# Kernel optimization log

Measured on AMD Instinct MI355X. Metric: run time of the kernel, lower is better.

The kernel has to match this reference:

```python
import jax, jax.numpy as jnp
import numpy as np

D_MODEL = 512
DK = 4
DV = 8
HIDD = 10
HEAD = D_MODEL // DV  # 64
LN_EPS = 1e-5


def setup_inputs() -> dict:
    key = jax.random.key(0)
    ks = jax.random.split(key, 10)
    B, S, Se = 8, 512, 512
    u = jax.random.uniform  # torch.rand initializer for attention weights
    n = jax.random.normal
    return {
        "x": n(ks[0], (B, S, D_MODEL), jnp.float32),
        "x_enc": n(ks[1], (B, Se, D_MODEL), jnp.float32),
        "WqM": u(ks[2], (D_MODEL, HEAD * DK), jnp.float32),
        "WkM": u(ks[3], (D_MODEL, HEAD * DK), jnp.float32),
        "WvM": u(ks[4], (D_MODEL, HEAD * DV), jnp.float32),
        "ln_g": jnp.ones((D_MODEL,), jnp.float32),
        "ln_b": jnp.zeros((D_MODEL,), jnp.float32),
        "fc1_w": n(ks[5], (HIDD, D_MODEL), jnp.float32) * (1.0 / np.sqrt(D_MODEL)),
        "fc1_b": jnp.zeros((HIDD,), jnp.float32),
        "fc2_w": n(ks[6], (D_MODEL, HIDD), jnp.float32) * (1.0 / np.sqrt(HIDD)),
        "fc2_b": jnp.zeros((D_MODEL,), jnp.float32),
    }


def _attention(Xq, Xkv, WqM, WkM, WvM, causal_mul_mask):
    # NOTE: cross-attention in the source also uses WqM/WkM/WvM (Wq/Wk/Wv unused).
    B, Sq, _ = Xq.shape
    Sk = Xkv.shape[1]
    Q = (Xq @ WqM).reshape(B, Sq, HEAD, DK)
    K = (Xkv @ WkM).reshape(B, Sk, HEAD, DK)
    V = (Xkv @ WvM).reshape(B, Sk, HEAD, DV)
    score = jnp.einsum('bqhd,bkhd->bhqk', Q, K) / np.sqrt(DK).astype(np.float32)
    if causal_mul_mask:
        # Faithful quirk: multiplicative tril mask on scores (NOT additive -inf).
        score = score * jnp.tril(jnp.ones((Sq, Sk), score.dtype))
    w = jax.nn.softmax(score, axis=-1)
    out = jnp.einsum('bhqk,bkhd->bqhd', w, V)
    return out.reshape(B, Sq, HEAD * DV)  # HEAD*DV == d_model


def _layernorm(x, g, b):
    mu = jnp.mean(x, axis=-1, keepdims=True)
    var = jnp.mean(jnp.square(x - mu), axis=-1, keepdims=True)
    return (x - mu) * jax.lax.rsqrt(var + LN_EPS) * g + b


def reference(x, x_enc, WqM, WkM, WvM, ln_g, ln_b, fc1_w, fc1_b, fc2_w, fc2_b):
    fx = _attention(x, x, WqM, WkM, WvM, causal_mul_mask=True)
    fx = _attention(fx, x_enc, WqM, WkM, WvM, causal_mul_mask=False)
    y = _layernorm(x + fx, ln_g, ln_b)
    h = jax.nn.relu(y @ fc1_w.T + fc1_b)
    return h @ fc2_w.T + fc2_b
```

## Files before the change

### kernel.cpp

```cpp
#include <hip/hip_runtime.h>
#include <math.h>

#define D_MODEL 512
#define BATCH 8
#define SEQ 512
#define HEAD 64
#define DK 4
#define DV 8
#define HIDD 10

#define MR 32
#define KC 64
#define NC 256

__global__ __launch_bounds__(256) void proj_kernel(
    const float* __restrict__ xq, const float* __restrict__ xkv,
    const float* __restrict__ Wq, const float* __restrict__ Wk,
    const float* __restrict__ Wv,
    float* __restrict__ Q, float* __restrict__ K, float* __restrict__ V)
{
    __shared__ float xt[KC * MR];
    __shared__ float wt[KC * NC];

    const int t  = threadIdx.x;
    const int bj = blockIdx.x & 3;
    const int br = blockIdx.x >> 2;
    const int r0 = br * MR;

    const float* X; const float* W; float* O; int ldw; int c0;
    if (bj == 0)      { X = xq;  W = Wq; O = Q; ldw = 256; c0 = 0;   }
    else if (bj == 1) { X = xkv; W = Wk; O = K; ldw = 256; c0 = 0;   }
    else if (bj == 2) { X = xkv; W = Wv; O = V; ldw = 512; c0 = 0;   }
    else              { X = xkv; W = Wv; O = V; ldw = 512; c0 = 256; }

    const int rg = t >> 6;
    const int cq = t & 63;

    float4 acc[8];
#pragma unroll
    for (int r = 0; r < 8; ++r) acc[r] = make_float4(0.f, 0.f, 0.f, 0.f);

    const int rs = t & 31;
    const int kq = t >> 5;

    for (int kc = 0; kc < D_MODEL; kc += KC) {
        const float4 xa = *(const float4*)(X + (long)(r0 + rs) * D_MODEL + kc + kq * 8);
        const float4 xb = *(const float4*)(X + (long)(r0 + rs) * D_MODEL + kc + kq * 8 + 4);
        xt[(kq * 8 + 0) * MR + rs] = xa.x;
        xt[(kq * 8 + 1) * MR + rs] = xa.y;
        xt[(kq * 8 + 2) * MR + rs] = xa.z;
        xt[(kq * 8 + 3) * MR + rs] = xa.w;
        xt[(kq * 8 + 4) * MR + rs] = xb.x;
        xt[(kq * 8 + 5) * MR + rs] = xb.y;
        xt[(kq * 8 + 6) * MR + rs] = xb.z;
        xt[(kq * 8 + 7) * MR + rs] = xb.w;

#pragma unroll
        for (int i = 0; i < 16; ++i) {
            const int row = i * 4 + rg;
            const float4 wv = *(const float4*)(W + (long)(kc + row) * ldw + c0 + cq * 4);
            *(float4*)(wt + row * NC + cq * 4) = wv;
        }
        __syncthreads();

#pragma unroll 4
        for (int k = 0; k < KC; ++k) {
            const float4 w4 = *(const float4*)(wt + k * NC + cq * 4);
            const float4 x0 = *(const float4*)(xt + k * MR + rg * 8);
            const float4 x1 = *(const float4*)(xt + k * MR + rg * 8 + 4);
            const float xr[8] = {x0.x, x0.y, x0.z, x0.w, x1.x, x1.y, x1.z, x1.w};
#pragma unroll
            for (int r = 0; r < 8; ++r) {
                acc[r].x = fmaf(xr[r], w4.x, acc[r].x);
                acc[r].y = fmaf(xr[r], w4.y, acc[r].y);
                acc[r].z = fmaf(xr[r], w4.z, acc[r].z);
                acc[r].w = fmaf(xr[r], w4.w, acc[r].w);
            }
        }
        __syncthreads();
    }

#pragma unroll
    for (int r = 0; r < 8; ++r) {
        const long row = r0 + rg * 8 + r;
        *(float4*)(O + row * ldw + c0 + cq * 4) = acc[r];
    }
}

__global__ __launch_bounds__(256) void attn_kernel(
    const float* __restrict__ Q, const float* __restrict__ K,
    const float* __restrict__ V, float* __restrict__ O, int causal)
{
    extern __shared__ float smem[];
    float* Kl = smem;
    float* Vl = smem + SEQ * DK;
    float* cs = Vl + SEQ * DV;

    const int t = threadIdx.x;
    const int bh = blockIdx.x >> 1;
    const int qhalf = blockIdx.x & 1;
    const int b = bh >> 6;
    const int h = bh & 63;

    const long kbase = (long)b * SEQ * 256 + h * DK;
    const long vbase = (long)b * SEQ * 512 + h * DV;
    for (int i = t; i < SEQ * DK; i += 256) {
        int s = i >> 2, d = i & 3;
        Kl[i] = K[kbase + (long)s * 256 + d];
    }
    for (int i = t; i < SEQ * DV; i += 256) {
        int s = i >> 3, d = i & 7;
        Vl[i] = V[vbase + (long)s * 512 + d];
    }
    __syncthreads();

    if (causal) {
        const int ch = t >> 3, d = t & 7;
        float s16 = 0.f;
#pragma unroll
        for (int i = 0; i < 16; ++i) s16 += Vl[(ch * 16 + i) * 8 + d];
        cs[ch * 8 + d] = s16;
        __syncthreads();
        if (t < 8) {
            cs[256 + t] = 0.f;
            float run = 0.f;
            for (int c2 = 31; c2 >= 0; --c2) {
                run += cs[c2 * 8 + t];
                cs[c2 * 8 + t] = run;
            }
        }
        __syncthreads();
    }

    const int q = qhalf * 256 + t;
    const long qbase = (long)b * SEQ * 256 + (long)q * 256 + h * DK;
    const float4 qv = *(const float4*)(Q + qbase);
    const float q0 = qv.x * 0.5f, q1 = qv.y * 0.5f;
    const float q2 = qv.z * 0.5f, q3 = qv.w * 0.5f;

    const int bound = causal ? q : (SEQ - 1);

    float m = -INFINITY, l = 0.f;
    float a0=0.f,a1=0.f,a2=0.f,a3=0.f,a4=0.f,a5=0.f,a6=0.f,a7=0.f;

    int s0 = 0;
    for (; s0 + 8 <= bound + 1; s0 += 8) {
        float sc[8];
#pragma unroll
        for (int i = 0; i < 8; ++i) {
            const float4 k4 = *(const float4*)(Kl + (s0 + i) * 4);
            sc[i] = fmaf(q0, k4.x, fmaf(q1, k4.y, fmaf(q2, k4.z, q3 * k4.w)));
        }
        float gm = fmaxf(fmaxf(fmaxf(sc[0], sc[1]), fmaxf(sc[2], sc[3])),
                         fmaxf(fmaxf(sc[4], sc[5]), fmaxf(sc[6], sc[7])));
        if (gm > m) {
            float scale = __expf(m - gm);
            l *= scale;
            a0*=scale; a1*=scale; a2*=scale; a3*=scale;
            a4*=scale; a5*=scale; a6*=scale; a7*=scale;
            m = gm;
        }
#pragma unroll
        for (int i = 0; i < 8; ++i) {
            float p = __expf(sc[i] - m);
            l += p;
            const float4 v0 = *(const float4*)(Vl + (s0 + i) * 8);
            const float4 v1 = *(const float4*)(Vl + (s0 + i) * 8 + 4);
            a0 = fmaf(p, v0.x, a0); a1 = fmaf(p, v0.y, a1);
            a2 = fmaf(p, v0.z, a2); a3 = fmaf(p, v0.w, a3);
            a4 = fmaf(p, v1.x, a4); a5 = fmaf(p, v1.y, a5);
            a6 = fmaf(p, v1.z, a6); a7 = fmaf(p, v1.w, a7);
        }
    }
    for (int s = s0; s <= bound; ++s) {
        const float4 k4 = *(const float4*)(Kl + s * 4);
        float sc = fmaf(q0, k4.x, fmaf(q1, k4.y, fmaf(q2, k4.z, q3 * k4.w)));
        if (sc > m) {
            float scale = __expf(m - sc);
            l *= scale;
            a0*=scale; a1*=scale; a2*=scale; a3*=scale;
            a4*=scale; a5*=scale; a6*=scale; a7*=scale;
            m = sc;
        }
        float p = __expf(sc - m);
        l += p;
        const float4 v0 = *(const float4*)(Vl + s * 8);
        const float4 v1 = *(const float4*)(Vl + s * 8 + 4);
        a0 = fmaf(p, v0.x, a0); a1 = fmaf(p, v0.y, a1);
        a2 = fmaf(p, v0.z, a2); a3 = fmaf(p, v0.w, a3);
        a4 = fmaf(p, v1.x, a4); a5 = fmaf(p, v1.y, a5);
        a6 = fmaf(p, v1.z, a6); a7 = fmaf(p, v1.w, a7);
    }

    if (causal && q < SEQ - 1) {
        float M = fmaxf(m, 0.f);
        float scale = __expf(m - M);
        float pm = __expf(-M);
        l = l * scale + pm * (float)(SEQ - 1 - q);
        int nq = q + 1;
        int cq2 = nq >> 4;
        float sv[8];
#pragma unroll
        for (int d = 0; d < 8; ++d) sv[d] = cs[(cq2 + 1) * 8 + d];
        for (int s = nq; s < (cq2 + 1) * 16; ++s) {
            const float4 v0 = *(const float4*)(Vl + s * 8);
            const float4 v1 = *(const float4*)(Vl + s * 8 + 4);
            sv[0]+=v0.x; sv[1]+=v0.y; sv[2]+=v0.z; sv[3]+=v0.w;
            sv[4]+=v1.x; sv[5]+=v1.y; sv[6]+=v1.z; sv[7]+=v1.w;
        }
        a0 = a0*scale + pm*sv[0]; a1 = a1*scale + pm*sv[1];
        a2 = a2*scale + pm*sv[2]; a3 = a3*scale + pm*sv[3];
        a4 = a4*scale + pm*sv[4]; a5 = a5*scale + pm*sv[5];
        a6 = a6*scale + pm*sv[6]; a7 = a7*scale + pm*sv[7];
    }

    float inv = 1.0f / l;
    const long obase = (long)b * SEQ * 512 + (long)q * 512 + h * DV;
    *(float4*)(O + obase)     = make_float4(a0*inv, a1*inv, a2*inv, a3*inv);
    *(float4*)(O + obase + 4) = make_float4(a4*inv, a5*inv, a6*inv, a7*inv);
}

__global__ __launch_bounds__(256) void ln_mlp_kernel(
    const float* __restrict__ x, const float* __restrict__ fx,
    const float* __restrict__ g, const float* __restrict__ beta,
    const float* __restrict__ w1, const float* __restrict__ b1,
    const float* __restrict__ w2, const float* __restrict__ b2,
    float* __restrict__ out)
{
    const int t = threadIdx.x;
    const int lane = t & 63;
    const int row = blockIdx.x * 4 + (t >> 6);
    const long base = (long)row * D_MODEL;
    const int e0 = lane * 8;

    const float4 xa = *(const float4*)(x + base + e0);
    const float4 xb = *(const float4*)(x + base + e0 + 4);
    const float4 fa = *(const float4*)(fx + base + e0);
    const float4 fb = *(const float4*)(fx + base + e0 + 4);
    float z[8] = {xa.x+fa.x, xa.y+fa.y, xa.z+fa.z, xa.w+fa.w,
                  xb.x+fb.x, xb.y+fb.y, xb.z+fb.z, xb.w+fb.w};

    float sum = 0.f;
#pragma unroll
    for (int j = 0; j < 8; ++j) sum += z[j];
#pragma unroll
    for (int o = 32; o > 0; o >>= 1) sum += __shfl_xor(sum, o);
    float mu = sum * (1.0f / 512.0f);

    float d[8], ss = 0.f;
#pragma unroll
    for (int j = 0; j < 8; ++j) { d[j] = z[j] - mu; ss += d[j] * d[j]; }
#pragma unroll
    for (int o = 32; o > 0; o >>= 1) ss += __shfl_xor(ss, o);
    float rs = rsqrtf(ss * (1.0f / 512.0f) + 1e-5f);

    const float4 ga = *(const float4*)(g + e0);
    const float4 gb = *(const float4*)(g + e0 + 4);
    const float4 ba = *(const float4*)(beta + e0);
    const float4 bb = *(const float4*)(beta + e0 + 4);
    const float gg[8] = {ga.x,ga.y,ga.z,ga.w,gb.x,gb.y,gb.z,gb.w};
    const float bt[8] = {ba.x,ba.y,ba.z,ba.w,bb.x,bb.y,bb.z,bb.w};
    float y[8];
#pragma unroll
    for (int j = 0; j < 8; ++j) y[j] = d[j] * rs * gg[j] + bt[j];

    float part[HIDD];
#pragma unroll
    for (int i = 0; i < HIDD; ++i) {
        const float4 wa = *(const float4*)(w1 + i * 512 + e0);
        const float4 wb = *(const float4*)(w1 + i * 512 + e0 + 4);
        part[i] = y[0]*wa.x + y[1]*wa.y + y[2]*wa.z + y[3]*wa.w
                + y[4]*wb.x + y[5]*wb.y + y[6]*wb.z + y[7]*wb.w;
    }
#pragma unroll
    for (int i = 0; i < HIDD; ++i)
#pragma unroll
        for (int o = 32; o > 0; o >>= 1) part[i] += __shfl_xor(part[i], o);

    float hv[HIDD];
#pragma unroll
    for (int i = 0; i < HIDD; ++i) hv[i] = fmaxf(part[i] + b1[i], 0.f);

    float o8[8];
#pragma unroll
    for (int j = 0; j < 8; ++j) o8[j] = b2[e0 + j];
#pragma unroll
    for (int i = 0; i < HIDD; ++i)
#pragma unroll
        for (int j = 0; j < 8; ++j)
            o8[j] = fmaf(hv[i], w2[(long)(e0 + j) * 10 + i], o8[j]);

    *(float4*)(out + base + e0)     = make_float4(o8[0], o8[1], o8[2], o8[3]);
    *(float4*)(out + base + e0 + 4) = make_float4(o8[4], o8[5], o8[6], o8[7]);
}

extern "C" void kernel_launch(void* const* d_in, const int* in_sizes, int n_in,
                              void* d_out, int out_size, void* d_ws, size_t ws_size,
                              hipStream_t stream) {
    (void)in_sizes; (void)n_in; (void)out_size; (void)ws_size;
    const float* x    = (const float*)d_in[0];
    const float* xenc = (const float*)d_in[1];
    const float* Wq   = (const float*)d_in[2];
    const float* Wk   = (const float*)d_in[3];
    const float* Wv   = (const float*)d_in[4];
    const float* ln_g = (const float*)d_in[5];
    const float* ln_b = (const float*)d_in[6];
    const float* w1   = (const float*)d_in[7];
    const float* b1   = (const float*)d_in[8];
    const float* w2   = (const float*)d_in[9];
    const float* b2   = (const float*)d_in[10];
    float* out = (float*)d_out;

    float* ws = (float*)d_ws;
    float* Q = ws;
    float* K = Q + 1048576;
    float* V = K + 1048576;
    float* A = V + 2097152;

    const int nrows = BATCH * SEQ;
    const size_t lds_cross  = (size_t)(SEQ * DK + SEQ * DV) * 4;
    const size_t lds_causal = lds_cross + (size_t)(33 * DV) * 4;
    const int proj_grid = (nrows / MR) * 4;

    proj_kernel<<<dim3(proj_grid), 256, 0, stream>>>(x, x, Wq, Wk, Wv, Q, K, V);
    attn_kernel<<<dim3(BATCH * HEAD * 2), 256, lds_causal, stream>>>(Q, K, V, A, 1);

    proj_kernel<<<dim3(proj_grid), 256, 0, stream>>>(A, xenc, Wq, Wk, Wv, Q, K, V);
    attn_kernel<<<dim3(BATCH * HEAD * 2), 256, lds_cross, stream>>>(Q, K, V, A, 0);

    ln_mlp_kernel<<<dim3(nrows / 4), 256, 0, stream>>>(x, A, ln_g, ln_b,
                                                       w1, b1, w2, b2, out);
}
```

Before: 356.0 us.

## Write Q/K/V in head-major layout and halve projection K-chunk

The projection kernel now stores Q, K and V in a per-(batch, head) contiguous layout instead of row-major. This lets the attention kernel load its K/V slices into LDS with coalesced float4 loads rather than strided scalar gathers. The projection k-chunk is also halved, which cuts LDS usage per block so more blocks can be resident, at the cost of more synchronisation rounds. The projection stores become strided instead of row-contiguous.

```diff
diff --git a/kernel.cpp b/kernel.cpp
--- a/kernel.cpp
+++ b/kernel.cpp
@@ -10,14 +10,14 @@
 #define HIDD 10
 
 #define MR 32
-#define KC 64
+#define KC 32
 #define NC 256
 
 __global__ __launch_bounds__(256) void proj_kernel(
     const float* __restrict__ xq, const float* __restrict__ xkv,
     const float* __restrict__ Wq, const float* __restrict__ Wk,
     const float* __restrict__ Wv,
-    float* __restrict__ Q, float* __restrict__ K, float* __restrict__ V)
+    float* __restrict__ Q2, float* __restrict__ K2, float* __restrict__ V2)
 {
     __shared__ float xt[KC * MR];
     __shared__ float wt[KC * NC];
@@ -27,39 +27,33 @@
     const int br = blockIdx.x >> 2;
     const int r0 = br * MR;
 
-    const float* X; const float* W; float* O; int ldw; int c0;
-    if (bj == 0)      { X = xq;  W = Wq; O = Q; ldw = 256; c0 = 0;   }
-    else if (bj == 1) { X = xkv; W = Wk; O = K; ldw = 256; c0 = 0;   }
-    else if (bj == 2) { X = xkv; W = Wv; O = V; ldw = 512; c0 = 0;   }
-    else              { X = xkv; W = Wv; O = V; ldw = 512; c0 = 256; }
+    const float* X; const float* W; int ldw; int c0;
+    if (bj == 0)      { X = xq;  W = Wq; ldw = 256; c0 = 0;   }
+    else if (bj == 1) { X = xkv; W = Wk; ldw = 256; c0 = 0;   }
+    else if (bj == 2) { X = xkv; W = Wv; ldw = 512; c0 = 0;   }
+    else              { X = xkv; W = Wv; ldw = 512; c0 = 256; }
 
     const int rg = t >> 6;
     const int cq = t & 63;
-
-    float4 acc[8];
-#pragma unroll
-    for (int r = 0; r < 8; ++r) acc[r] = make_float4(0.f, 0.f, 0.f, 0.f);
-
     const int rs = t & 31;
     const int kq = t >> 5;
 
+    float4 acc[8];
+#pragma unroll
+    for (int r = 0; r < 8; ++r) acc[r] = make_float4(0.f, 0.f, 0.f, 0.f);
+
     for (int kc = 0; kc < D_MODEL; kc += KC) {
-        const float4 xa = *(const float4*)(X + (long)(r0 + rs) * D_MODEL + kc + kq * 8);
-        const float4 xb = *(const float4*)(X + (long)(r0 + rs) * D_MODEL + kc + kq * 8 + 4);
-        xt[(kq * 8 + 0) * MR + rs] = xa.x;
-        xt[(kq * 8 + 1) * MR + rs] = xa.y;
-        xt[(kq * 8 + 2) * MR + rs] = xa.z;
-        xt[(kq * 8 + 3) * MR + rs] = xa.w;
-        xt[(kq * 8 + 4) * MR + rs] = xb.x;
-        xt[(kq * 8 + 5) * MR + rs] = xb.y;
-        xt[(kq * 8 + 6) * MR + rs] = xb.z;
-        xt[(kq * 8 + 7) * MR + rs] = xb.w;
-
-#pragma unroll
-        for (int i = 0; i < 16; ++i) {
+        const float4 xa = *(const float4*)(X + (long)(r0 + rs) * D_MODEL + kc + kq * 4);
+        xt[(kq * 4 + 0) * MR + rs] = xa.x;
+        xt[(kq * 4 + 1) * MR + rs] = xa.y;
+        xt[(kq * 4 + 2) * MR + rs] = xa.z;
+        xt[(kq * 4 + 3) * MR + rs] = xa.w;
+
+#pragma unroll
+        for (int i = 0; i < 8; ++i) {
             const int row = i * 4 + rg;
-            const float4 wv = *(const float4*)(W + (long)(kc + row) * ldw + c0 + cq * 4);
-            *(float4*)(wt + row * NC + cq * 4) = wv;
+            *(float4*)(wt + row * NC + cq * 4) =
+                *(const float4*)(W + (long)(kc + row) * ldw + c0 + cq * 4);
         }
         __syncthreads();
 
@@ -80,16 +74,26 @@
         __syncthreads();
     }
 
-#pragma unroll
-    for (int r = 0; r < 8; ++r) {
-        const long row = r0 + rg * 8 + r;
-        *(float4*)(O + row * ldw + c0 + cq * 4) = acc[r];
+    const int b = r0 >> 9;
+    const int sb = (r0 & 511) + rg * 8;
+    if (bj <= 1) {
+        float* dst = (bj == 0) ? Q2 : K2;
+#pragma unroll
+        for (int r = 0; r < 8; ++r)
+            *(float4*)(dst + (((long)b * HEAD + cq) * SEQ + sb + r) * 4) = acc[r];
+    } else {
+        const int col = c0 + cq * 4;
+        const int h = col >> 3;
+        const int off = col & 7;
+#pragma unroll
+        for (int r = 0; r < 8; ++r)
+            *(float4*)(V2 + (((long)b * HEAD + h) * SEQ + sb + r) * 8 + off) = acc[r];
     }
 }
 
 __global__ __launch_bounds__(256) void attn_kernel(
-    const float* __restrict__ Q, const float* __restrict__ K,
-    const float* __restrict__ V, float* __restrict__ O, int causal)
+    const float* __restrict__ Q2, const float* __restrict__ K2,
+    const float* __restrict__ V2, float* __restrict__ O, int causal)
 {
     extern __shared__ float smem[];
     float* Kl = smem;
@@ -102,16 +106,13 @@
     const int b = bh >> 6;
     const int h = bh & 63;
 
-    const long kbase = (long)b * SEQ * 256 + h * DK;
-    const long vbase = (long)b * SEQ * 512 + h * DV;
-    for (int i = t; i < SEQ * DK; i += 256) {
-        int s = i >> 2, d = i & 3;
-        Kl[i] = K[kbase + (long)s * 256 + d];
-    }
-    for (int i = t; i < SEQ * DV; i += 256) {
-        int s = i >> 3, d = i & 7;
-        Vl[i] = V[vbase + (long)s * 512 + d];
-    }
+    const float4* Ks = (const float4*)(K2 + (long)bh * SEQ * DK);
+    ((float4*)Kl)[t]       = Ks[t];
+    ((float4*)Kl)[t + 256] = Ks[t + 256];
+    const float4* Vs = (const float4*)(V2 + (long)bh * SEQ * DV);
+#pragma unroll
+    for (int i = 0; i < 4; ++i)
+        ((float4*)Vl)[t + i * 256] = Vs[t + i * 256];
     __syncthreads();
 
     if (causal) {
@@ -133,8 +134,7 @@
     }
 
     const int q = qhalf * 256 + t;
-    const long qbase = (long)b * SEQ * 256 + (long)q * 256 + h * DK;
-    const float4 qv = *(const float4*)(Q + qbase);
+    const float4 qv = *(const float4*)(Q2 + ((long)bh * SEQ + q) * 4);
     const float q0 = qv.x * 0.5f, q1 = qv.y * 0.5f;
     const float q2 = qv.z * 0.5f, q3 = qv.w * 0.5f;
 
@@ -312,21 +312,21 @@
     float* out = (float*)d_out;
 
     float* ws = (float*)d_ws;
-    float* Q = ws;
-    float* K = Q + 1048576;
-    float* V = K + 1048576;
-    float* A = V + 2097152;
+    float* Q2 = ws;
+    float* K2 = Q2 + 1048576;
+    float* V2 = K2 + 1048576;
+    float* A  = V2 + 2097152;
 
     const int nrows = BATCH * SEQ;
     const size_t lds_cross  = (size_t)(SEQ * DK + SEQ * DV) * 4;
     const size_t lds_causal = lds_cross + (size_t)(33 * DV) * 4;
     const int proj_grid = (nrows / MR) * 4;
 
-    proj_kernel<<<dim3(proj_grid), 256, 0, stream>>>(x, x, Wq, Wk, Wv, Q, K, V);
-    attn_kernel<<<dim3(BATCH * HEAD * 2), 256, lds_causal, stream>>>(Q, K, V, A, 1);
-
-    proj_kernel<<<dim3(proj_grid), 256, 0, stream>>>(A, xenc, Wq, Wk, Wv, Q, K, V);
-    attn_kernel<<<dim3(BATCH * HEAD * 2), 256, lds_cross, stream>>>(Q, K, V, A, 0);
+    proj_kernel<<<dim3(proj_grid), 256, 0, stream>>>(x, x, Wq, Wk, Wv, Q2, K2, V2);
+    attn_kernel<<<dim3(BATCH * HEAD * 2), 256, lds_causal, stream>>>(Q2, K2, V2, A, 1);
+
+    proj_kernel<<<dim3(proj_grid), 256, 0, stream>>>(A, xenc, Wq, Wk, Wv, Q2, K2, V2);
+    attn_kernel<<<dim3(BATCH * HEAD * 2), 256, lds_cross, stream>>>(Q2, K2, V2, A, 0);
 
     ln_mlp_kernel<<<dim3(nrows / 4), 256, 0, stream>>>(x, A, ln_g, ln_b,
                                                        w1, b1, w2, b2, out);
```

Result: faster. 340.8 us (-4.3%).
